# Kernel tuning notes

Measured on AMD Instinct MI355X. Metric: run time of the kernel, lower is better.

Reference implementation:

```python
import jax, jax.numpy as jnp
import numpy as np

EMBED = 1024
HEADS = 16
HEAD_DIM = EMBED // HEADS
SCALING = HEAD_DIM ** -0.5
R = 16
LORA_SCALE = 32.0 / R  # alpha / r
NEG = jnp.finfo(jnp.float32).min


def lora_linear(x, W, A, B):
    # y = x @ W.T + (x @ A.T) @ B.T * scale   (LinearLora, bias=False)
    return x @ W.T + ((x @ A.T) @ B.T) * LORA_SCALE


def setup_inputs() -> dict:
    key = jax.random.key(0)
    ks = jax.random.split(key, 14)
    B, T, D = 1, 4096, EMBED
    hidden_states = jax.random.normal(ks[0], (B, T, D), jnp.float32)
    # causal additive mask (bsz, 1, tgt, src): 0 on/below diag, dtype-min above
    i = jnp.arange(T)
    causal = jnp.where(i[:, None] >= i[None, :], 0.0, NEG).astype(jnp.float32)
    attention_mask = jnp.broadcast_to(causal, (B, 1, T, T))
    s = 0.02
    def w(k, shape):
        return jax.random.normal(k, shape, jnp.float32) * s
    return dict(
        hidden_states=hidden_states,
        attention_mask=attention_mask,
        Wq=w(ks[1], (D, D)), Wk=w(ks[2], (D, D)), Wv=w(ks[3], (D, D)), Wo=w(ks[4], (D, D)),
        Aq=w(ks[5], (R, D)), Bq=jnp.zeros((D, R), jnp.float32) + w(ks[6], (D, R)),
        Ak=w(ks[7], (R, D)), Bk=w(ks[8], (D, R)),
        Av=w(ks[9], (R, D)), Bv=w(ks[10], (D, R)),
        Ao=w(ks[11], (R, D)), Bo=w(ks[12], (D, R)),
    )


def reference(hidden_states, attention_mask, Wq, Wk, Wv, Wo,
              Aq, Bq, Ak, Bk, Av, Bv, Ao, Bo):
    bsz, tgt_len, _ = hidden_states.shape
    H, Hd = HEADS, HEAD_DIM

    q = lora_linear(hidden_states, Wq, Aq, Bq) * SCALING
    k = lora_linear(hidden_states, Wk, Ak, Bk)
    v = lora_linear(hidden_states, Wv, Av, Bv)

    # (b, t, H, Hd)
    q = q.reshape(bsz, tgt_len, H, Hd)
    k = k.reshape(bsz, tgt_len, H, Hd)
    v = v.reshape(bsz, tgt_len, H, Hd)

    # scores (b, H, t, s)
    attn = jnp.einsum('bthd,bshd->bhts', q, k)
    attn = attn + attention_mask
    attn = jnp.maximum(attn, NEG)
    attn = jax.nn.softmax(attn, axis=-1)  # dropout p=0 / eval mode

    out = jnp.einsum('bhts,bshd->bthd', attn, v)
    out = out.reshape(bsz, tgt_len, H * Hd)
    out = lora_linear(out, Wo, Ao, Bo)
    return out
```

## Files before the change

kernel.cpp:

```cpp
#include <hip/hip_runtime.h>
#include <cmath>
#include <cstdint>

typedef unsigned short u16;
typedef __attribute__((ext_vector_type(8))) __bf16 bf16x8;
typedef __attribute__((ext_vector_type(4))) __bf16 bf16x4;
typedef __attribute__((ext_vector_type(4))) short s16x4;
typedef __attribute__((ext_vector_type(4))) float f32x4;

__device__ __forceinline__ u16 f2bf(float f) {
    union { float f; unsigned u; } v; v.f = f;
    unsigned r = v.u + 0x7fffu + ((v.u >> 16) & 1u);
    return (u16)(r >> 16);
}

__device__ __forceinline__ void gload_lds(const u16* g, u16* l) {
    __builtin_amdgcn_global_load_lds((__attribute__((address_space(1))) void*)g,
                                     (__attribute__((address_space(3))) void*)l,
                                     16, 0, 0);
}

__device__ __forceinline__ f32x4 mfma16(s16x4 a, s16x4 b, f32x4 c) {
#if __has_builtin(__builtin_amdgcn_mfma_f32_16x16x16bf16_1k)
    return __builtin_amdgcn_mfma_f32_16x16x16bf16_1k(a, b, c, 0, 0, 0);
#else
    asm("v_mfma_f32_16x16x16_bf16 %0, %1, %2, %3"
        : "=v"(c) : "v"(a), "v"(b), "0"(c));
    return c;
#endif
}

__global__ __launch_bounds__(256) void prep_all(
        const float* __restrict__ X,
        const float* __restrict__ Wq, const float* __restrict__ Wk,
        const float* __restrict__ Wv, const float* __restrict__ Wo,
        const float* __restrict__ Aq, const float* __restrict__ Bq,
        const float* __restrict__ Ak, const float* __restrict__ Bk,
        const float* __restrict__ Av, const float* __restrict__ Bv,
        const float* __restrict__ Ao, const float* __restrict__ Bo,
        u16* __restrict__ Wqkv, u16* __restrict__ Wob, u16* __restrict__ Xb) {
    const int p = blockIdx.y;
    const int idx = blockIdx.x * 256 + threadIdx.x;
    if (p == 4) {
        float4 v = ((const float4*)X)[idx];
        ushort4 o;
        o.x = f2bf(v.x); o.y = f2bf(v.y); o.z = f2bf(v.z); o.w = f2bf(v.w);
        ((ushort4*)Xb)[idx] = o;
        return;
    }
    const int n = idx >> 10, d = idx & 1023;
    const float* W; const float* A; const float* B;
    switch (p) {
        case 0: W = Wq; A = Aq; B = Bq; break;
        case 1: W = Wk; A = Ak; B = Bk; break;
        case 2: W = Wv; A = Av; B = Bv; break;
        default: W = Wo; A = Ao; B = Bo; break;
    }
    float lora = 0.f;
#pragma unroll
    for (int r = 0; r < 16; r++) lora += B[n * 16 + r] * A[r * 1024 + d];
    float v = W[idx] + 2.0f * lora;
    if (p == 0) v *= 0.125f * 1.44269504088896340736f;
    if (p < 3) Wqkv[(size_t)p * 1048576 + idx] = f2bf(v);
    else       Wob[idx] = f2bf(v);
}

template <bool F32OUT>
__global__ __launch_bounds__(256, 3) void gemm_bt(const u16* __restrict__ A,
                                                  const u16* __restrict__ B,
                                                  void* __restrict__ C, int ldc) {
    __shared__ __align__(16) u16 As[128 * 64];
    __shared__ __align__(16) u16 Bs[128 * 64];
    const int tid = threadIdx.x;
    const int lane = tid & 63, wave = tid >> 6;
    const int quad = lane >> 4, l16 = lane & 15;
    const int wm = (wave >> 1) * 64, wn = (wave & 1) * 64;
    const size_t m0 = (size_t)blockIdx.y * 128, n0 = (size_t)blockIdx.x * 128;
    const u16* Ap = A + m0 * 1024;
    const u16* Bp = B + n0 * 1024;
    const int xsw = l16 & 7;
    f32x4 acc[4][4] = {};
    for (int k0 = 0; k0 < 1024; k0 += 64) {
#pragma unroll
        for (int hh = 0; hh < 4; hh++) {
            int c = tid + hh * 256;
            int row = c >> 3, cg = (c & 7) ^ (row & 7);
            gload_lds(Ap + (size_t)row * 1024 + k0 + cg * 8, As + c * 8);
            gload_lds(Bp + (size_t)row * 1024 + k0 + cg * 8, Bs + c * 8);
        }
        asm volatile("s_waitcnt vmcnt(0)" ::: "memory");
        __syncthreads();
#pragma unroll
        for (int kf = 0; kf < 2; kf++) {
            bf16x8 af[4], bfr[4];
#pragma unroll
            for (int i = 0; i < 4; i++) {
                af[i]  = *(const bf16x8*)(As + (wm + i * 16 + l16) * 64
                                             + ((kf * 4 + quad) ^ xsw) * 8);
                bfr[i] = *(const bf16x8*)(Bs + (wn + i * 16 + l16) * 64
                                             + ((kf * 4 + quad) ^ xsw) * 8);
            }
#pragma unroll
            for (int mi = 0; mi < 4; mi++)
#pragma unroll
                for (int ni = 0; ni < 4; ni++)
                    acc[mi][ni] = __builtin_amdgcn_mfma_f32_16x16x32_bf16(
                            af[mi], bfr[ni], acc[mi][ni], 0, 0, 0);
        }
        __syncthreads();
    }
#pragma unroll
    for (int mi = 0; mi < 4; mi++)
#pragma unroll
        for (int ni = 0; ni < 4; ni++)
#pragma unroll
            for (int r = 0; r < 4; r++) {
                size_t row = m0 + wm + mi * 16 + quad * 4 + r;
                size_t col = n0 + wn + ni * 16 + l16;
                if (F32OUT) ((float*)C)[row * ldc + col] = acc[mi][ni][r];
                else        ((u16*)C)[row * ldc + col] = f2bf(acc[mi][ni][r]);
            }
}

template <bool F32OUT>
__global__ __launch_bounds__(256, 3) void gemm_bt64(const u16* __restrict__ A,
                                                    const u16* __restrict__ B,
                                                    void* __restrict__ C, int ldc) {
    __shared__ __align__(16) u16 As[64 * 64];
    __shared__ __align__(16) u16 Bs[128 * 64];
    const int tid = threadIdx.x;
    const int lane = tid & 63, wave = tid >> 6;
    const int quad = lane >> 4, l16 = lane & 15;
    const int wm = (wave >> 1) * 32, wn = (wave & 1) * 64;
    const size_t m0 = (size_t)blockIdx.y * 64, n0 = (size_t)blockIdx.x * 128;
    const u16* Ap = A + m0 * 1024;
    const u16* Bp = B + n0 * 1024;
    const int xsw = l16 & 7;
    f32x4 acc[2][4] = {};
    for (int k0 = 0; k0 < 1024; k0 += 64) {
#pragma unroll
        for (int hh = 0; hh < 2; hh++) {
            int c = tid + hh * 256;
            int row = c >> 3, cg = (c & 7) ^ (row & 7);
            gload_lds(Ap + (size_t)row * 1024 + k0 + cg * 8, As + c * 8);
        }
#pragma unroll
        for (int hh = 0; hh < 4; hh++) {
            int c = tid + hh * 256;
            int row = c >> 3, cg = (c & 7) ^ (row & 7);
            gload_lds(Bp + (size_t)row * 1024 + k0 + cg * 8, Bs + c * 8);
        }
        asm volatile("s_waitcnt vmcnt(0)" ::: "memory");
        __syncthreads();
#pragma unroll
        for (int kf = 0; kf < 2; kf++) {
            bf16x8 af[2], bfr[4];
#pragma unroll
            for (int i = 0; i < 2; i++)
                af[i] = *(const bf16x8*)(As + (wm + i * 16 + l16) * 64
                                            + ((kf * 4 + quad) ^ xsw) * 8);
#pragma unroll
            for (int i = 0; i < 4; i++)
                bfr[i] = *(const bf16x8*)(Bs + (wn + i * 16 + l16) * 64
                                             + ((kf * 4 + quad) ^ xsw) * 8);
#pragma unroll
            for (int mi = 0; mi < 2; mi++)
#pragma unroll
                for (int ni = 0; ni < 4; ni++)
                    acc[mi][ni] = __builtin_amdgcn_mfma_f32_16x16x32_bf16(
                            af[mi], bfr[ni], acc[mi][ni], 0, 0, 0);
        }
        __syncthreads();
    }
#pragma unroll
    for (int mi = 0; mi < 2; mi++)
#pragma unroll
        for (int ni = 0; ni < 4; ni++)
#pragma unroll
            for (int r = 0; r < 4; r++) {
                size_t row = m0 + wm + mi * 16 + quad * 4 + r;
                size_t col = n0 + wn + ni * 16 + l16;
                if (F32OUT) ((float*)C)[row * ldc + col] = acc[mi][ni][r];
                else        ((u16*)C)[row * ldc + col] = f2bf(acc[mi][ni][r]);
            }
}

__global__ __launch_bounds__(256) void transpose_v(const u16* __restrict__ Y,
                                                   u16* __restrict__ Vt) {
    __shared__ u16 tile[64][68];
    const int dv0 = blockIdx.x * 64;
    const int t0  = blockIdx.y * 64;
    const int tid = threadIdx.x;
#pragma unroll
    for (int p = 0; p < 4; p++) {
        int pos = tid + p * 256;
        int row = pos >> 4;
        int c4  = (pos & 15) * 4;
        ushort4 v = *(const ushort4*)(Y + (size_t)(t0 + row) * 3072 + 2048 + dv0 + c4);
        tile[row][c4 + 0] = v.x; tile[row][c4 + 1] = v.y;
        tile[row][c4 + 2] = v.z; tile[row][c4 + 3] = v.w;
    }
    __syncthreads();
#pragma unroll
    for (int p = 0; p < 4; p++) {
        int pos = tid + p * 256;
        int orow = pos >> 4;
        int oc4  = (pos & 15) * 4;
        ushort4 o;
        o.x = tile[oc4 + 0][orow]; o.y = tile[oc4 + 1][orow];
        o.z = tile[oc4 + 2][orow]; o.w = tile[oc4 + 3][orow];
        *(ushort4*)(Vt + (size_t)(dv0 + orow) * 4096 + t0 + oc4) = o;
    }
}

__global__ __launch_bounds__(256, 4) void flash_attn(
        const u16* __restrict__ Y,
        const u16* __restrict__ Vt,
        u16* __restrict__ O,
        float* __restrict__ OpA,
        float* __restrict__ OpB,
        float* __restrict__ lA,
        float* __restrict__ lB) {
    __shared__ __align__(16) u16 lds[16384];
    const int tid = threadIdx.x;
    const int wave = tid >> 6, lane = tid & 63;
    const int quad = lane >> 4, l16 = lane & 15;
    const int bid = blockIdx.x;
    const int g = bid >> 4, h = bid & 15;
    int p, t0, t1, mode;
    if (g < 32)      { p = 32 + g;  t0 = 0;  t1 = 32;    mode = 1; }
    else if (g < 64) { p = 63 - g;  t0 = 0;  t1 = p + 1; mode = 0; }
    else             { p = 127 - g; t0 = 32; t1 = p + 1; mode = 2; }
    const int q0w = p * 64 + wave * 16;
    const u16* Kbase = Y + 1024 + h * 64;
    const u16* Vbase = Vt + (size_t)(h * 64) * 4096;
    const int xsw = l16 & 7;

    bf16x8 qf[2];
#pragma unroll
    for (int kf = 0; kf < 2; kf++)
        qf[kf] = *(const bf16x8*)(Y + (size_t)(q0w + l16) * 3072
                                    + h * 64 + kf * 32 + quad * 8);

    f32x4 oaccT[4] = {};
    f32x4 lacc = {};
    const s16x4 ones = { (short)0x3F80, (short)0x3F80,
                         (short)0x3F80, (short)0x3F80 };

    {
        const int s0p = t0 * 64;
        u16* Kn = lds + (t0 & 1) * 8192;
#pragma unroll
        for (int pp = 0; pp < 2; pp++) {
            int c = pp * 256 + tid;
            int row = c >> 3, cg = (c & 7) ^ (row & 7);
            gload_lds(Kbase + (size_t)(s0p + row) * 3072 + cg * 8, Kn + c * 8);
            gload_lds(Vbase + (size_t)row * 4096 + s0p + cg * 8, Kn + 4096 + c * 8);
        }
    }

#pragma unroll 1
    for (int t = t0; t < t1; t++) {
        const int s0 = t * 64;
        u16* Ks = lds + (t & 1) * 8192;
        u16* Vs = Ks + 4096;
        asm volatile("s_waitcnt vmcnt(0)" ::: "memory");
        __syncthreads();

        if (t + 1 < t1) {
            u16* Kn = lds + ((t + 1) & 1) * 8192;
            const int sn = s0 + 64;
#pragma unroll
            for (int pp = 0; pp < 2; pp++) {
                int c = pp * 256 + tid;
                int row = c >> 3, cg = (c & 7) ^ (row & 7);
                gload_lds(Kbase + (size_t)(sn + row) * 3072 + cg * 8, Kn + c * 8);
                gload_lds(Vbase + (size_t)row * 4096 + sn + cg * 8, Kn + 4096 + c * 8);
            }
        }

        bf16x8 kfr[4][2];
#pragma unroll
        for (int ni = 0; ni < 4; ni++) {
            int row = ni * 16 + l16;
            kfr[ni][0] = *(const bf16x8*)(Ks + row * 64 + ((quad) ^ xsw) * 8);
            kfr[ni][1] = *(const bf16x8*)(Ks + row * 64 + ((4 + quad) ^ xsw) * 8);
        }

        f32x4 sacc[4] = {};
#pragma unroll
        for (int ni = 0; ni < 4; ni++) {
            sacc[ni] = __builtin_amdgcn_mfma_f32_16x16x32_bf16(
                    kfr[ni][0], qf[0], sacc[ni], 0, 0, 0);
            sacc[ni] = __builtin_amdgcn_mfma_f32_16x16x32_bf16(
                    kfr[ni][1], qf[1], sacc[ni], 0, 0, 0);
        }

        s16x4 vfr[4][4];
#pragma unroll
        for (int nj = 0; nj < 4; nj++) {
            int row = nj * 16 + l16;
#pragma unroll
            for (int ni = 0; ni < 4; ni++) {
                int cc = ni * 2 + (quad >> 1);
                vfr[nj][ni] = *(const s16x4*)(Vs + row * 64 + (cc ^ xsw) * 8
                                                 + (quad & 1) * 4);
            }
        }

        const int qg = q0w + l16;
        const bool diag = (t == p);
#pragma unroll
        for (int ni = 0; ni < 4; ni++) {
            if (diag) {
#pragma unroll
                for (int r = 0; r < 4; r++) {
                    int sg = s0 + ni * 16 + quad * 4 + r;
                    if (sg > qg) sacc[ni][r] = -INFINITY;
                }
            }
            f32x4 pe;
#pragma unroll
            for (int r = 0; r < 4; r++)
                pe[r] = __builtin_amdgcn_exp2f(sacc[ni][r]);
            bf16x4 tt = { (__bf16)pe[0], (__bf16)pe[1],
                          (__bf16)pe[2], (__bf16)pe[3] };
            s16x4 pf = __builtin_bit_cast(s16x4, tt);
            lacc = mfma16(ones, pf, lacc);
#pragma unroll
            for (int nj = 0; nj < 4; nj++)
                oaccT[nj] = mfma16(vfr[nj][ni], pf, oaccT[nj]);
        }
    }

    __syncthreads();
    if (mode == 0) {
        u16* scr = lds + wave * 1152;
        float inv = 1.0f / lacc[0];
#pragma unroll
        for (int nj = 0; nj < 4; nj++) {
            bf16x4 t4 = { (__bf16)(oaccT[nj][0] * inv),
                          (__bf16)(oaccT[nj][1] * inv),
                          (__bf16)(oaccT[nj][2] * inv),
                          (__bf16)(oaccT[nj][3] * inv) };
            *(s16x4*)(scr + l16 * 72 + nj * 16 + quad * 4) =
                    __builtin_bit_cast(s16x4, t4);
        }
        asm volatile("s_waitcnt lgkmcnt(0)" ::: "memory");
#pragma unroll
        for (int pp = 0; pp < 2; pp++) {
            int row = pp * 8 + (lane >> 3);
            int seg = (lane & 7) * 8;
            bf16x8 d = *(const bf16x8*)(scr + row * 72 + seg);
            *(bf16x8*)(O + (size_t)(q0w + row) * 1024 + h * 64 + seg) = d;
        }
    } else {
        float* Op = (mode == 1) ? OpA : OpB;
        float* lp = (mode == 1) ? lA : lB;
        float* scr = (float*)lds + wave * 1088;
#pragma unroll
        for (int nj = 0; nj < 4; nj++)
            *(f32x4*)(scr + l16 * 68 + nj * 16 + quad * 4) = oaccT[nj];
        asm volatile("s_waitcnt lgkmcnt(0)" ::: "memory");
#pragma unroll
        for (int it = 0; it < 4; it++) {
            int row = (lane >> 4) + it * 4;
            int seg = (lane & 15) * 4;
            f32x4 d = *(const f32x4*)(scr + row * 68 + seg);
            *(f32x4*)(Op + (size_t)(q0w + row - 2048) * 1024 + h * 64 + seg) = d;
        }
        if (lane < 16)
            lp[(size_t)(q0w + lane - 2048) * 16 + h] = lacc[0];
    }
}

__global__ __launch_bounds__(256) void combine_o(
        const float* __restrict__ OpA, const float* __restrict__ OpB,
        const float* __restrict__ lA, const float* __restrict__ lB,
        u16* __restrict__ O) {
    const int idx = blockIdx.x * 256 + threadIdx.x;
    const int r = idx >> 7;
    const int c8 = (idx & 127) * 8;
    const int h = c8 >> 6;
    const float inv = 1.0f / (lA[r * 16 + h] + lB[r * 16 + h]);
    const float* a = OpA + (size_t)r * 1024 + c8;
    const float* b = OpB + (size_t)r * 1024 + c8;
    float4 a0 = *(const float4*)a, a1 = *(const float4*)(a + 4);
    float4 b0 = *(const float4*)b, b1 = *(const float4*)(b + 4);
    ushort4 o0, o1;
    o0.x = f2bf((a0.x + b0.x) * inv); o0.y = f2bf((a0.y + b0.y) * inv);
    o0.z = f2bf((a0.z + b0.z) * inv); o0.w = f2bf((a0.w + b0.w) * inv);
    o1.x = f2bf((a1.x + b1.x) * inv); o1.y = f2bf((a1.y + b1.y) * inv);
    o1.z = f2bf((a1.z + b1.z) * inv); o1.w = f2bf((a1.w + b1.w) * inv);
    u16* op = O + (size_t)(2048 + r) * 1024 + c8;
    *(ushort4*)op = o0;
    *(ushort4*)(op + 4) = o1;
}


extern "C" void kernel_launch(void* const* d_in, const int* in_sizes, int n_in,
                              void* d_out, int out_size, void* d_ws, size_t ws_size,
                              hipStream_t stream) {
    const float* X  = (const float*)d_in[0];
    const float* Wq = (const float*)d_in[2];
    const float* Wk = (const float*)d_in[3];
    const float* Wv = (const float*)d_in[4];
    const float* Wo = (const float*)d_in[5];
    const float* Aq = (const float*)d_in[6];
    const float* Bq = (const float*)d_in[7];
    const float* Ak = (const float*)d_in[8];
    const float* Bk = (const float*)d_in[9];
    const float* Av = (const float*)d_in[10];
    const float* Bv = (const float*)d_in[11];
    const float* Ao = (const float*)d_in[12];
    const float* Bo = (const float*)d_in[13];

    char* ws = (char*)d_ws;
    u16*   Xb   = (u16*)(ws);
    float* OpA  = (float*)(ws);
    u16*   Wqkv = (u16*)(ws + (8u  << 20));
    float* OpB  = (float*)(ws + (8u  << 20));
    float* lA   = (float*)(ws + (16u << 20));
    float* lB   = (float*)(ws + (16u << 20) + (128u << 10));
    u16*   Y    = (u16*)(ws + (17u << 20));
    u16*   Vt   = (u16*)(ws + (41u << 20));
    u16*   Ob   = (u16*)(ws + (49u << 20));
    u16*   Wob  = (u16*)(ws + (57u << 20));

    prep_all<<<dim3(4096, 5), 256, 0, stream>>>(X, Wq, Wk, Wv, Wo, Aq, Bq, Ak, Bk,
                                                Av, Bv, Ao, Bo, Wqkv, Wob, Xb);
    gemm_bt<false><<<dim3(24, 32), 256, 0, stream>>>(Xb, Wqkv, Y, 3072);
    transpose_v<<<dim3(16, 64), 256, 0, stream>>>(Y, Vt);
    flash_attn<<<dim3(1536), 256, 0, stream>>>(Y, Vt, Ob, OpA, OpB, lA, lB);
    combine_o<<<dim3(1024), 256, 0, stream>>>(OpA, OpB, lA, lB, Ob);
    gemm_bt64<true><<<dim3(8, 64), 256, 0, stream>>>(Ob, Wob, d_out, 1024);
}
```

Measured before the change: 270.2 us.

## Double per-wave query rows in flash attention with a static block schedule

Each wave now handles 32 query rows (two 16-row halves) instead of 16, so every K/V tile loaded into LDS feeds twice as many MFMAs, and each block covers 128 query rows. The grid shrinks to 768 blocks, and a hand-ordered lookup table assigns each block its row group and split mode (whole, first half, second half) so long causal jobs start first. Launch bounds drop to 3 blocks per CU to make room for the doubled accumulators, and the workspace is rearranged. The cost is fewer resident waves for hiding latency and more register pressure.

```diff
diff --git a/kernel.cpp b/kernel.cpp
--- a/kernel.cpp
+++ b/kernel.cpp
@@ -213,7 +213,16 @@
     }
 }
 
-__global__ __launch_bounds__(256, 4) void flash_attn(
+__device__ const unsigned char SCHED[48] = {
+    (1<<6)|31, (0<<6)|15, (1<<6)|30, (2<<6)|30, (2<<6)|29, (0<<6)|14, (2<<6)|28, (1<<6)|27,
+    (2<<6)|27, (0<<6)|13, (2<<6)|26, (2<<6)|25, (0<<6)|12, (1<<6)|24, (2<<6)|24, (2<<6)|23,
+    (2<<6)|31, (1<<6)|29, (1<<6)|28, (1<<6)|26, (1<<6)|25, (1<<6)|23, (1<<6)|22, (1<<6)|21,
+    (1<<6)|20, (2<<6)|20, (1<<6)|19, (2<<6)|19, (2<<6)|21, (2<<6)|22, (0<<6)|10, (0<<6)|11,
+    (0<<6)|0,  (0<<6)|1,  (0<<6)|2,  (0<<6)|3,  (0<<6)|4,  (0<<6)|5,  (0<<6)|6,  (0<<6)|7,
+    (1<<6)|16, (2<<6)|16, (1<<6)|18, (0<<6)|9,  (1<<6)|17, (2<<6)|17, (2<<6)|18, (0<<6)|8
+};
+
+__global__ __launch_bounds__(256, 3) void flash_attn(
         const u16* __restrict__ Y,
         const u16* __restrict__ Vt,
         u16* __restrict__ O,
@@ -227,23 +236,25 @@
     const int quad = lane >> 4, l16 = lane & 15;
     const int bid = blockIdx.x;
     const int g = bid >> 4, h = bid & 15;
-    int p, t0, t1, mode;
-    if (g < 32)      { p = 32 + g;  t0 = 0;  t1 = 32;    mode = 1; }
-    else if (g < 64) { p = 63 - g;  t0 = 0;  t1 = p + 1; mode = 0; }
-    else             { p = 127 - g; t0 = 32; t1 = p + 1; mode = 2; }
-    const int q0w = p * 64 + wave * 16;
+    const int sc = SCHED[g];
+    const int p = sc & 63, mode = sc >> 6;
+    const int t0 = (mode == 2) ? p + 1 : 0;
+    const int t1 = (mode == 1) ? p + 1 : 2 * p + 2;
+    const int q0w = p * 128 + wave * 32;
     const u16* Kbase = Y + 1024 + h * 64;
     const u16* Vbase = Vt + (size_t)(h * 64) * 4096;
     const int xsw = l16 & 7;
 
-    bf16x8 qf[2];
-#pragma unroll
-    for (int kf = 0; kf < 2; kf++)
-        qf[kf] = *(const bf16x8*)(Y + (size_t)(q0w + l16) * 3072
-                                    + h * 64 + kf * 32 + quad * 8);
-
-    f32x4 oaccT[4] = {};
-    f32x4 lacc = {};
+    bf16x8 qf[2][2];
+#pragma unroll
+    for (int qh = 0; qh < 2; qh++)
+#pragma unroll
+        for (int kf = 0; kf < 2; kf++)
+            qf[qh][kf] = *(const bf16x8*)(Y + (size_t)(q0w + qh * 16 + l16) * 3072
+                                            + h * 64 + kf * 32 + quad * 8);
+
+    f32x4 oaccT[2][4] = {};
+    f32x4 lacc[2] = {};
     const s16x4 ones = { (short)0x3F80, (short)0x3F80,
                          (short)0x3F80, (short)0x3F80 };
 
@@ -286,16 +297,6 @@
             kfr[ni][0] = *(const bf16x8*)(Ks + row * 64 + ((quad) ^ xsw) * 8);
             kfr[ni][1] = *(const bf16x8*)(Ks + row * 64 + ((4 + quad) ^ xsw) * 8);
         }
-
-        f32x4 sacc[4] = {};
-#pragma unroll
-        for (int ni = 0; ni < 4; ni++) {
-            sacc[ni] = __builtin_amdgcn_mfma_f32_16x16x32_bf16(
-                    kfr[ni][0], qf[0], sacc[ni], 0, 0, 0);
-            sacc[ni] = __builtin_amdgcn_mfma_f32_16x16x32_bf16(
-                    kfr[ni][1], qf[1], sacc[ni], 0, 0, 0);
-        }
-
         s16x4 vfr[4][4];
 #pragma unroll
         for (int nj = 0; nj < 4; nj++) {
@@ -308,69 +309,89 @@
             }
         }
 
-        const int qg = q0w + l16;
-        const bool diag = (t == p);
-#pragma unroll
-        for (int ni = 0; ni < 4; ni++) {
-            if (diag) {
-#pragma unroll
-                for (int r = 0; r < 4; r++) {
-                    int sg = s0 + ni * 16 + quad * 4 + r;
-                    if (sg > qg) sacc[ni][r] = -INFINITY;
+        const bool diag = (t >= 2 * p);
+#pragma unroll
+        for (int qh = 0; qh < 2; qh++) {
+            f32x4 sacc[4] = {};
+#pragma unroll
+            for (int ni = 0; ni < 4; ni++) {
+                sacc[ni] = __builtin_amdgcn_mfma_f32_16x16x32_bf16(
+                        kfr[ni][0], qf[qh][0], sacc[ni], 0, 0, 0);
+                sacc[ni] = __builtin_amdgcn_mfma_f32_16x16x32_bf16(
+                        kfr[ni][1], qf[qh][1], sacc[ni], 0, 0, 0);
+            }
+            const int qg = q0w + qh * 16 + l16;
+#pragma unroll
+            for (int ni = 0; ni < 4; ni++) {
+                if (diag) {
+#pragma unroll
+                    for (int r = 0; r < 4; r++) {
+                        int sg = s0 + ni * 16 + quad * 4 + r;
+                        if (sg > qg) sacc[ni][r] = -INFINITY;
+                    }
                 }
-            }
-            f32x4 pe;
-#pragma unroll
-            for (int r = 0; r < 4; r++)
-                pe[r] = __builtin_amdgcn_exp2f(sacc[ni][r]);
-            bf16x4 tt = { (__bf16)pe[0], (__bf16)pe[1],
-                          (__bf16)pe[2], (__bf16)pe[3] };
-            s16x4 pf = __builtin_bit_cast(s16x4, tt);
-            lacc = mfma16(ones, pf, lacc);
-#pragma unroll
-            for (int nj = 0; nj < 4; nj++)
-                oaccT[nj] = mfma16(vfr[nj][ni], pf, oaccT[nj]);
+                f32x4 pe;
+#pragma unroll
+                for (int r = 0; r < 4; r++)
+                    pe[r] = __builtin_amdgcn_exp2f(sacc[ni][r]);
+                bf16x4 tt = { (__bf16)pe[0], (__bf16)pe[1],
+                              (__bf16)pe[2], (__bf16)pe[3] };
+                s16x4 pf = __builtin_bit_cast(s16x4, tt);
+                lacc[qh] = mfma16(ones, pf, lacc[qh]);
+#pragma unroll
+                for (int nj = 0; nj < 4; nj++)
+                    oaccT[qh][nj] = mfma16(vfr[nj][ni], pf, oaccT[qh][nj]);
+            }
         }
     }
 
     __syncthreads();
     if (mode == 0) {
         u16* scr = lds + wave * 1152;
-        float inv = 1.0f / lacc[0];
-#pragma unroll
-        for (int nj = 0; nj < 4; nj++) {
-            bf16x4 t4 = { (__bf16)(oaccT[nj][0] * inv),
-                          (__bf16)(oaccT[nj][1] * inv),
-                          (__bf16)(oaccT[nj][2] * inv),
-                          (__bf16)(oaccT[nj][3] * inv) };
-            *(s16x4*)(scr + l16 * 72 + nj * 16 + quad * 4) =
-                    __builtin_bit_cast(s16x4, t4);
-        }
-        asm volatile("s_waitcnt lgkmcnt(0)" ::: "memory");
-#pragma unroll
-        for (int pp = 0; pp < 2; pp++) {
-            int row = pp * 8 + (lane >> 3);
-            int seg = (lane & 7) * 8;
-            bf16x8 d = *(const bf16x8*)(scr + row * 72 + seg);
-            *(bf16x8*)(O + (size_t)(q0w + row) * 1024 + h * 64 + seg) = d;
+#pragma unroll 1
+        for (int qh = 0; qh < 2; qh++) {
+            float inv = 1.0f / lacc[qh][0];
+#pragma unroll
+            for (int nj = 0; nj < 4; nj++) {
+                bf16x4 t4 = { (__bf16)(oaccT[qh][nj][0] * inv),
+                              (__bf16)(oaccT[qh][nj][1] * inv),
+                              (__bf16)(oaccT[qh][nj][2] * inv),
+                              (__bf16)(oaccT[qh][nj][3] * inv) };
+                *(s16x4*)(scr + l16 * 72 + nj * 16 + quad * 4) =
+                        __builtin_bit_cast(s16x4, t4);
+            }
+            asm volatile("s_waitcnt lgkmcnt(0)" ::: "memory");
+#pragma unroll
+            for (int pp = 0; pp < 2; pp++) {
+                int row = pp * 8 + (lane >> 3);
+                int seg = (lane & 7) * 8;
+                bf16x8 d = *(const bf16x8*)(scr + row * 72 + seg);
+                *(bf16x8*)(O + (size_t)(q0w + qh * 16 + row) * 1024 + h * 64 + seg) = d;
+            }
+            asm volatile("s_waitcnt lgkmcnt(0)" ::: "memory");
         }
     } else {
         float* Op = (mode == 1) ? OpA : OpB;
         float* lp = (mode == 1) ? lA : lB;
         float* scr = (float*)lds + wave * 1088;
-#pragma unroll
-        for (int nj = 0; nj < 4; nj++)
-            *(f32x4*)(scr + l16 * 68 + nj * 16 + quad * 4) = oaccT[nj];
-        asm volatile("s_waitcnt lgkmcnt(0)" ::: "memory");
-#pragma unroll
-        for (int it = 0; it < 4; it++) {
-            int row = (lane >> 4) + it * 4;
-            int seg = (lane & 15) * 4;
-            f32x4 d = *(const f32x4*)(scr + row * 68 + seg);
-            *(f32x4*)(Op + (size_t)(q0w + row - 2048) * 1024 + h * 64 + seg) = d;
-        }
-        if (lane < 16)
-            lp[(size_t)(q0w + lane - 2048) * 16 + h] = lacc[0];
+#pragma unroll 1
+        for (int qh = 0; qh < 2; qh++) {
+#pragma unroll
+            for (int nj = 0; nj < 4; nj++)
+                *(f32x4*)(scr + l16 * 68 + nj * 16 + quad * 4) = oaccT[qh][nj];
+            asm volatile("s_waitcnt lgkmcnt(0)" ::: "memory");
+#pragma unroll
+            for (int it = 0; it < 4; it++) {
+                int row = (lane >> 4) + it * 4;
+                int seg = (lane & 15) * 4;
+                f32x4 d = *(const f32x4*)(scr + row * 68 + seg);
+                *(f32x4*)(Op + (size_t)(q0w + qh * 16 + row - 2048) * 1024
+                             + h * 64 + seg) = d;
+            }
+            if (lane < 16)
+                lp[(size_t)(q0w + qh * 16 + lane - 2048) * 16 + h] = lacc[qh][0];
+            asm volatile("s_waitcnt lgkmcnt(0)" ::: "memory");
+        }
     }
 }
 
@@ -420,18 +441,18 @@
     float* OpA  = (float*)(ws);
     u16*   Wqkv = (u16*)(ws + (8u  << 20));
     float* OpB  = (float*)(ws + (8u  << 20));
-    float* lA   = (float*)(ws + (16u << 20));
-    float* lB   = (float*)(ws + (16u << 20) + (128u << 10));
-    u16*   Y    = (u16*)(ws + (17u << 20));
-    u16*   Vt   = (u16*)(ws + (41u << 20));
-    u16*   Ob   = (u16*)(ws + (49u << 20));
-    u16*   Wob  = (u16*)(ws + (57u << 20));
+    u16*   Y    = (u16*)(ws + (16u << 20));
+    u16*   Vt   = (u16*)(ws + (40u << 20));
+    u16*   Ob   = (u16*)(ws + (48u << 20));
+    u16*   Wob  = (u16*)(ws + (56u << 20));
+    float* lA   = (float*)(ws + (58u << 20));
+    float* lB   = (float*)(ws + (58u << 20) + (128u << 10));
 
     prep_all<<<dim3(4096, 5), 256, 0, stream>>>(X, Wq, Wk, Wv, Wo, Aq, Bq, Ak, Bk,
                                                 Av, Bv, Ao, Bo, Wqkv, Wob, Xb);
     gemm_bt<false><<<dim3(24, 32), 256, 0, stream>>>(Xb, Wqkv, Y, 3072);
     transpose_v<<<dim3(16, 64), 256, 0, stream>>>(Y, Vt);
-    flash_attn<<<dim3(1536), 256, 0, stream>>>(Y, Vt, Ob, OpA, OpB, lA, lB);
+    flash_attn<<<dim3(768), 256, 0, stream>>>(Y, Vt, Ob, OpA, OpB, lA, lB);
     combine_o<<<dim3(1024), 256, 0, stream>>>(OpA, OpB, lA, lB, Ob);
     gemm_bt64<true><<<dim3(8, 64), 256, 0, stream>>>(Ob, Wob, d_out, 1024);
 }
```

After: 392.4 us. 45.2% more time.
